# Kernel optimization log

Hardware: AMD Instinct MI355X
Metric: run time of the kernel (lower is better)

Reference implementation:

```python
import jax, jax.numpy as jnp
import numpy as np
from math import sqrt

B, N, D = 8, 4096, 512

def rotary(x, phases):
    # x: [B,N,D], phases: [B,N,D/2]
    c, s = jnp.cos(phases), jnp.sin(phases)
    a, b = jnp.split(x, 2, axis=-1)
    return jnp.concatenate([a * c - b * s, a * s + b * c], axis=-1)

def setup_inputs() -> dict:
    key = jax.random.key(0)
    ks = jax.random.split(key, 8)
    phi = jax.random.normal(ks[0], (B, N, D), dtype=jnp.float32)
    coords = jax.random.normal(ks[1], (B, N, 3), dtype=jnp.float32)
    weights = jax.random.uniform(ks[2], (B, N), dtype=jnp.float32)
    std = 1.0 / sqrt(D)
    Wq = jax.random.normal(ks[3], (D, D), dtype=jnp.float32) * std
    Wk = jax.random.normal(ks[4], (D, D), dtype=jnp.float32) * std
    Wv = jax.random.normal(ks[5], (D, D), dtype=jnp.float32) * std
    bq = jnp.zeros((D,), jnp.float32)
    bk = jnp.zeros((D,), jnp.float32)
    bv = jnp.zeros((D,), jnp.float32)
    # mode_lift weight, std = 1/kernel_scale with kernel_scale=1.0
    Wrot = jax.random.normal(ks[6], (D // 2, 3), dtype=jnp.float32)
    return {"phi": phi, "coords": coords, "weights": weights,
            "Wq": Wq, "bq": bq, "Wk": Wk, "bk": bk, "Wv": Wv, "bv": bv,
            "Wrot": Wrot}

def reference(phi, coords, weights, Wq, bq, Wk, bk, Wv, bv, Wrot):
    d = phi.shape[-1]
    q = phi @ Wq.T + bq
    k = phi @ Wk.T + bk
    v = phi @ Wv.T + bv
    # _normalize: scale query by 1/sqrt(d); attach quadrature weights to value
    q = q * (1.0 / sqrt(d))
    v = weights[..., None] * v
    # rotary positional encoding on q and k
    phases = jnp.einsum('bnc,dc->bnd', coords, Wrot)  # [B,N,D/2]
    q = rotary(q, phases)
    k = rotary(k, phases)
    # linear attention: q @ (k^T @ v), O(N*d^2)
    kv = jnp.einsum('bnd,bne->bde', k, v)   # [B,D,D]
    return jnp.einsum('bnd,bde->bne', q, kv)  # [B,N,D]
```

## Files before the change

### kernel.cpp

```cpp
#include <hip/hip_runtime.h>


typedef _Float16 f16x8 __attribute__((ext_vector_type(8)));
typedef _Float16 f16x4 __attribute__((ext_vector_type(4)));
typedef float f32x4 __attribute__((ext_vector_type(4)));

__device__ __forceinline__ void gl_lds16(const void* g, void* l) {
    __builtin_amdgcn_global_load_lds(
        (const __attribute__((address_space(1))) void*)g,
        (__attribute__((address_space(3))) void*)l, 16, 0, 0);
}

__device__ __forceinline__ void stage2(const _Float16* gA, size_t sA,
                                       const _Float16* gB, size_t sB,
                                       _Float16* As, _Float16* Bs,
                                       int ca, int srow, int sseg) {
    gl_lds16(&gA[(size_t)(ca * 16 + srow) * sA + sseg], &As[ca * 512]);
    gl_lds16(&gA[(size_t)(ca * 16 + 16 + srow) * sA + sseg], &As[(ca + 1) * 512]);
    gl_lds16(&gB[(size_t)(ca * 16 + srow) * sB + sseg], &Bs[ca * 512]);
    gl_lds16(&gB[(size_t)(ca * 16 + 16 + srow) * sB + sseg], &Bs[(ca + 1) * 512]);
}

__device__ __forceinline__ void mfma_step(const _Float16* As, const _Float16* Bs,
                                          int wm, int wn, int l16, int quad,
                                          f32x4 acc[4][4]) {
    f16x8 af[4], bf[4];
    #pragma unroll
    for (int mi = 0; mi < 4; mi++)
        af[mi] = *(const f16x8*)&As[(wm + mi * 16 + l16) * 32 + quad * 8];
    #pragma unroll
    for (int ni = 0; ni < 4; ni++)
        bf[ni] = *(const f16x8*)&Bs[(wn + ni * 16 + l16) * 32 + quad * 8];
    #pragma unroll
    for (int mi = 0; mi < 4; mi++)
        #pragma unroll
        for (int ni = 0; ni < 4; ni++)
            acc[mi][ni] = __builtin_amdgcn_mfma_f32_16x16x32_f16(
                af[mi], bf[ni], acc[mi][ni], 0, 0, 0);
}

__global__ __launch_bounds__(256) void convert_phi(const float* __restrict__ phi,
                                                   _Float16* __restrict__ phi_h) {
    int i = (blockIdx.x * 256 + threadIdx.x) * 4;
    float4 v = *(const float4*)(phi + i);
    f16x4 o = {(_Float16)v.x, (_Float16)v.y, (_Float16)v.z, (_Float16)v.w};
    *(f16x4*)(phi_h + i) = o;
}

__global__ __launch_bounds__(256) void pack_w(
    const float* __restrict__ Wq, const float* __restrict__ Wk,
    const float* __restrict__ Wv, const float* __restrict__ bq,
    const float* __restrict__ bk, const float* __restrict__ bv,
    _Float16* __restrict__ wcat, float* __restrict__ bcat) {
    int j = blockIdx.x;
    int reg = j >> 9, jr = j & 511;
    const float* W; const float* bias;
    if (reg == 0)      { W = Wq; bias = bq; }
    else if (reg == 1) { W = Wk; bias = bk; }
    else               { W = Wv; bias = bv; }
    int d = (reg < 2) ? ((jr & 1) ? (jr >> 1) + 256 : (jr >> 1)) : jr;
    for (int i = threadIdx.x; i < 512; i += 256)
        wcat[j * 512 + i] = (_Float16)W[d * 512 + i];
    if (threadIdx.x == 0) bcat[j] = bias[d];
}

__global__ __launch_bounds__(256) void qkv_kernel(
    const _Float16* __restrict__ phi_h, const _Float16* __restrict__ wcat,
    const float* __restrict__ bcat, const float* __restrict__ coords,
    const float* __restrict__ weights, const float* __restrict__ Wrot,
    _Float16* __restrict__ qr, _Float16* __restrict__ krT,
    _Float16* __restrict__ vwT) {
    __shared__ __align__(16) char smem[34816];
    _Float16* As0 = (_Float16*)smem;
    _Float16* Bs0 = (_Float16*)(smem + 8192);
    _Float16* As1 = (_Float16*)(smem + 16384);
    _Float16* Bs1 = (_Float16*)(smem + 24576);
    _Float16* Ts  = (_Float16*)smem;

    const int tid = threadIdx.x;
    const int lane = tid & 63, wave = tid >> 6;
    const int quad = lane >> 4, l16 = lane & 15;
    const int wm = (wave >> 1) * 64, wn = (wave & 1) * 64;
    const int m0 = blockIdx.y * 128;
    const int c0 = blockIdx.x * 128;
    const int ca = wave * 2;
    const int srow = lane >> 2, sseg = (lane & 3) * 8;

    const _Float16* gA = phi_h + (size_t)m0 * 512;
    const _Float16* gB = wcat + (size_t)c0 * 512;

    f32x4 acc[4][4] = {};

    stage2(gA, 512, gB, 512, As0, Bs0, ca, srow, sseg);
    __syncthreads();
    for (int k0 = 0; k0 < 512; k0 += 64) {
        stage2(gA + k0 + 32, 512, gB + k0 + 32, 512, As1, Bs1, ca, srow, sseg);
        mfma_step(As0, Bs0, wm, wn, l16, quad, acc);
        __syncthreads();
        if (k0 + 64 < 512)
            stage2(gA + k0 + 64, 512, gB + k0 + 64, 512, As0, Bs0, ca, srow, sseg);
        mfma_step(As1, Bs1, wm, wn, l16, quad, acc);
        __syncthreads();
    }

    const int region = c0 >> 9;
    const float qscale = 0.04419417382415922f;

    float bias[4], w0[4], w1[4], w2[4];
    #pragma unroll
    for (int ni = 0; ni < 4; ni++) {
        int gc = c0 + wn + ni * 16 + l16;
        bias[ni] = bcat[gc];
        if (region < 2) {
            int jp = (gc & 511) >> 1;
            w0[ni] = Wrot[jp * 3];
            w1[ni] = Wrot[jp * 3 + 1];
            w2[ni] = Wrot[jp * 3 + 2];
        }
    }

    if (region == 0) {
        #pragma unroll
        for (int mi = 0; mi < 4; mi++)
            #pragma unroll
            for (int r = 0; r < 4; r++) {
                int row = wm + mi * 16 + quad * 4 + r;
                int gm = m0 + row;
                float x = coords[gm * 3], y = coords[gm * 3 + 1], z = coords[gm * 3 + 2];
                #pragma unroll
                for (int ni = 0; ni < 4; ni++) {
                    float val = (acc[mi][ni][r] + bias[ni]) * qscale;
                    float part = __shfl_xor(val, 1);
                    float ph = x * w0[ni] + y * w1[ni] + z * w2[ni];
                    float sv, cv; __sincosf(ph, &sv, &cv);
                    float res = (l16 & 1) ? (part * sv + val * cv)
                                          : (val * cv - part * sv);
                    Ts[row * 136 + wn + ni * 16 + l16] = (_Float16)res;
                }
            }
        __syncthreads();
        for (int i = tid; i < 2048; i += 256) {
            int row = i >> 4, cv = (i & 15) * 8;
            *(f16x8*)&qr[(m0 + row) * 512 + c0 + cv] = *(f16x8*)&Ts[row * 136 + cv];
        }
    } else {
        #pragma unroll
        for (int mi = 0; mi < 4; mi++)
            #pragma unroll
            for (int r = 0; r < 4; r++) {
                int row = wm + mi * 16 + quad * 4 + r;
                int gm = m0 + row;
                if (region == 1) {
                    float x = coords[gm * 3], y = coords[gm * 3 + 1], z = coords[gm * 3 + 2];
                    #pragma unroll
                    for (int ni = 0; ni < 4; ni++) {
                        float val = acc[mi][ni][r] + bias[ni];
                        float part = __shfl_xor(val, 1);
                        float ph = x * w0[ni] + y * w1[ni] + z * w2[ni];
                        float sv, cv; __sincosf(ph, &sv, &cv);
                        float res = (l16 & 1) ? (part * sv + val * cv)
                                              : (val * cv - part * sv);
                        Ts[(wn + ni * 16 + l16) * 136 + row] = (_Float16)res;
                    }
                } else {
                    float wgt = weights[gm];
                    #pragma unroll
                    for (int ni = 0; ni < 4; ni++) {
                        float val = (acc[mi][ni][r] + bias[ni]) * wgt;
                        Ts[(wn + ni * 16 + l16) * 136 + row] = (_Float16)val;
                    }
                }
            }
        __syncthreads();
        _Float16* dst = (region == 1) ? krT : vwT;
        const int b = m0 >> 12, n0 = m0 & 4095, cb = c0 & 511;
        for (int i = tid; i < 2048; i += 256) {
            int col = i >> 4, rv = (i & 15) * 8;
            *(f16x8*)&dst[((size_t)b * 512 + cb + col) * 4096 + n0 + rv] =
                *(f16x8*)&Ts[col * 136 + rv];
        }
    }
}

__global__ __launch_bounds__(256) void kv_kernel(
    const _Float16* __restrict__ vwT, const _Float16* __restrict__ krT,
    _Float16* __restrict__ kvp) {
    __shared__ __align__(16) char smem[32768];
    _Float16* As0 = (_Float16*)smem;
    _Float16* Bs0 = (_Float16*)(smem + 8192);
    _Float16* As1 = (_Float16*)(smem + 16384);
    _Float16* Bs1 = (_Float16*)(smem + 24576);
    const int tid = threadIdx.x, lane = tid & 63, wave = tid >> 6;
    const int quad = lane >> 4, l16 = lane & 15;
    const int wm = (wave >> 1) * 64, wn = (wave & 1) * 64;
    const int d0 = blockIdx.x * 128, e0 = blockIdx.y * 128;
    const int b = blockIdx.z >> 3, split = blockIdx.z & 7;
    const int ca = wave * 2;
    const int srow = lane >> 2, sseg = (lane & 3) * 8;
    const size_t base = (size_t)b * 512 * 4096;
    const int kbeg = split * 512;
    const _Float16* gA = vwT + base + (size_t)e0 * 4096 + kbeg;
    const _Float16* gB = krT + base + (size_t)d0 * 4096 + kbeg;
    f32x4 acc[4][4] = {};

    stage2(gA, 4096, gB, 4096, As0, Bs0, ca, srow, sseg);
    __syncthreads();
    for (int k0 = 0; k0 < 512; k0 += 64) {
        stage2(gA + k0 + 32, 4096, gB + k0 + 32, 4096, As1, Bs1, ca, srow, sseg);
        mfma_step(As0, Bs0, wm, wn, l16, quad, acc);
        __syncthreads();
        if (k0 + 64 < 512)
            stage2(gA + k0 + 64, 4096, gB + k0 + 64, 4096, As0, Bs0, ca, srow, sseg);
        mfma_step(As1, Bs1, wm, wn, l16, quad, acc);
        __syncthreads();
    }

    _Float16* dst = kvp + ((size_t)split * 8 + b) * 262144;
    #pragma unroll
    for (int mi = 0; mi < 4; mi++)
        #pragma unroll
        for (int ni = 0; ni < 4; ni++)
            #pragma unroll
            for (int r = 0; r < 4; r++) {
                int e = e0 + wm + mi * 16 + quad * 4 + r;
                int d = d0 + wn + ni * 16 + l16;
                dst[e * 512 + d] = (_Float16)acc[mi][ni][r];
            }
}

__global__ __launch_bounds__(256) void reduce_kv(const _Float16* __restrict__ kvp,
                                                 _Float16* __restrict__ kvT) {
    int i = (blockIdx.x * 256 + threadIdx.x) * 8;
    float s[8] = {};
    #pragma unroll
    for (int sp = 0; sp < 8; sp++) {
        f16x8 v = *(const f16x8*)(kvp + (size_t)sp * 2097152 + i);
        #pragma unroll
        for (int j = 0; j < 8; j++) s[j] += (float)v[j];
    }
    f16x8 o;
    #pragma unroll
    for (int j = 0; j < 8; j++) o[j] = (_Float16)s[j];
    *(f16x8*)(kvT + i) = o;
}

__global__ __launch_bounds__(256) void out_kernel(
    const _Float16* __restrict__ qr, const _Float16* __restrict__ kvT,
    float* __restrict__ out) {
    __shared__ __align__(16) char smem[32768];
    _Float16* As0 = (_Float16*)smem;
    _Float16* Bs0 = (_Float16*)(smem + 8192);
    _Float16* As1 = (_Float16*)(smem + 16384);
    _Float16* Bs1 = (_Float16*)(smem + 24576);
    const int tid = threadIdx.x, lane = tid & 63, wave = tid >> 6;
    const int quad = lane >> 4, l16 = lane & 15;
    const int wm = (wave >> 1) * 64, wn = (wave & 1) * 64;
    const int m0 = blockIdx.y * 128, e0 = blockIdx.x * 128;
    const int b = m0 >> 12;
    const int ca = wave * 2;
    const int srow = lane >> 2, sseg = (lane & 3) * 8;
    const _Float16* gA = qr + (size_t)m0 * 512;
    const _Float16* gB = kvT + (size_t)b * 262144 + (size_t)e0 * 512;
    f32x4 acc[4][4] = {};

    stage2(gA, 512, gB, 512, As0, Bs0, ca, srow, sseg);
    __syncthreads();
    for (int k0 = 0; k0 < 512; k0 += 64) {
        stage2(gA + k0 + 32, 512, gB + k0 + 32, 512, As1, Bs1, ca, srow, sseg);
        mfma_step(As0, Bs0, wm, wn, l16, quad, acc);
        __syncthreads();
        if (k0 + 64 < 512)
            stage2(gA + k0 + 64, 512, gB + k0 + 64, 512, As0, Bs0, ca, srow, sseg);
        mfma_step(As1, Bs1, wm, wn, l16, quad, acc);
        __syncthreads();
    }

    #pragma unroll
    for (int mi = 0; mi < 4; mi++)
        #pragma unroll
        for (int ni = 0; ni < 4; ni++)
            #pragma unroll
            for (int r = 0; r < 4; r++) {
                int gm = m0 + wm + mi * 16 + quad * 4 + r;
                int e = e0 + wn + ni * 16 + l16;
                out[(size_t)gm * 512 + e] = acc[mi][ni][r];
            }
}

extern "C" void kernel_launch(void* const* d_in, const int* in_sizes, int n_in,
                              void* d_out, int out_size, void* d_ws, size_t ws_size,
                              hipStream_t stream) {
    const float* phi     = (const float*)d_in[0];
    const float* coords  = (const float*)d_in[1];
    const float* weights = (const float*)d_in[2];
    const float* Wq      = (const float*)d_in[3];
    const float* bq      = (const float*)d_in[4];
    const float* Wk      = (const float*)d_in[5];
    const float* bk      = (const float*)d_in[6];
    const float* Wv      = (const float*)d_in[7];
    const float* bv      = (const float*)d_in[8];
    const float* Wrot    = (const float*)d_in[9];
    float* out = (float*)d_out;

    char* ws = (char*)d_ws;
    _Float16* phi_h = (_Float16*)(ws);
    _Float16* kvp   = (_Float16*)(ws);
    _Float16* wcat  = (_Float16*)(ws + 33554432);
    float*    bcat  = (float*)   (ws + 35127296);
    _Float16* qr    = (_Float16*)(ws + 35133440);
    _Float16* krT   = (_Float16*)(ws + 68687872);
    _Float16* vwT   = (_Float16*)(ws + 102242304);
    _Float16* kvT   = (_Float16*)(ws + 135796736);

    convert_phi<<<16384, 256, 0, stream>>>(phi, phi_h);
    pack_w<<<1536, 256, 0, stream>>>(Wq, Wk, Wv, bq, bk, bv, wcat, bcat);
    qkv_kernel<<<dim3(12, 256), 256, 0, stream>>>(phi_h, wcat, bcat, coords,
                                                  weights, Wrot, qr, krT, vwT);
    kv_kernel<<<dim3(4, 4, 64), 256, 0, stream>>>(vwT, krT, kvp);
    reduce_kv<<<1024, 256, 0, stream>>>(kvp, kvT);
    out_kernel<<<dim3(4, 256), 256, 0, stream>>>(qr, kvT, out);
}
```

Before: 322.4 us.

## Swizzle LDS tiles and use vmcnt-gated double-buffer pipeline in GEMMs

Applies an XOR swizzle to the 16-byte segment index used by the global-to-LDS staging loads and the MFMA fragment reads, to reduce LDS bank conflicts. It also replaces the __syncthreads-based double-buffer loop with a fully unrolled pipeline. That pipeline issues two stages ahead, waits on vmcnt for only the oldest stage, and uses raw s_barrier with sched_barrier fences. The aim is to keep global loads in flight across MFMA steps. The hand-written waitcnt and barrier ordering adds fragility if the vmcnt count does not match the number of outstanding loads.

Result: faster. 310.9 us (-3.6%).

```diff
diff --git a/kernel.cpp b/kernel.cpp
--- a/kernel.cpp
+++ b/kernel.cpp
@@ -22,15 +22,15 @@
 }
 
 __device__ __forceinline__ void mfma_step(const _Float16* As, const _Float16* Bs,
-                                          int wm, int wn, int l16, int quad,
+                                          int wm, int wn, int l16, int qs,
                                           f32x4 acc[4][4]) {
     f16x8 af[4], bf[4];
     #pragma unroll
     for (int mi = 0; mi < 4; mi++)
-        af[mi] = *(const f16x8*)&As[(wm + mi * 16 + l16) * 32 + quad * 8];
+        af[mi] = *(const f16x8*)&As[(wm + mi * 16 + l16) * 32 + qs * 8];
     #pragma unroll
     for (int ni = 0; ni < 4; ni++)
-        bf[ni] = *(const f16x8*)&Bs[(wn + ni * 16 + l16) * 32 + quad * 8];
+        bf[ni] = *(const f16x8*)&Bs[(wn + ni * 16 + l16) * 32 + qs * 8];
     #pragma unroll
     for (int mi = 0; mi < 4; mi++)
         #pragma unroll
@@ -38,6 +38,36 @@
             acc[mi][ni] = __builtin_amdgcn_mfma_f32_16x16x32_f16(
                 af[mi], bf[ni], acc[mi][ni], 0, 0, 0);
 }
+
+#define PHASE(BUFA, BUFB, VM)                                                 \
+    asm volatile("s_waitcnt vmcnt(" #VM ")" ::: "memory");                    \
+    __builtin_amdgcn_s_barrier();                                             \
+    asm volatile("" ::: "memory");                                            \
+    __builtin_amdgcn_sched_barrier(0);                                        \
+    mfma_step(BUFA, BUFB, wm, wn, l16, qs, acc);                              \
+    asm volatile("s_waitcnt lgkmcnt(0)" ::: "memory");                        \
+    __builtin_amdgcn_sched_barrier(0);                                        \
+    __builtin_amdgcn_s_barrier();                                             \
+    asm volatile("" ::: "memory");
+
+#define PIPE_LOOP(gA, sA, gB, sB)                                             \
+    stage2(gA, sA, gB, sB, As0, Bs0, ca, srow, sseg);                         \
+    stage2(gA + 32, sA, gB + 32, sB, As1, Bs1, ca, srow, sseg);               \
+    _Pragma("unroll")                                                         \
+    for (int p = 0; p < 8; p++) {                                             \
+        const int t0 = 2 * p;                                                 \
+        PHASE(As0, Bs0, 4)                                                    \
+        if (t0 + 2 < 16)                                                      \
+            stage2(gA + (size_t)(t0 + 2) * 32, sA,                            \
+                   gB + (size_t)(t0 + 2) * 32, sB,                            \
+                   As0, Bs0, ca, srow, sseg);                                 \
+        if (p < 7) { PHASE(As1, Bs1, 4) }                                     \
+        else       { PHASE(As1, Bs1, 0) }                                     \
+        if (t0 + 3 < 16)                                                      \
+            stage2(gA + (size_t)(t0 + 3) * 32, sA,                            \
+                   gB + (size_t)(t0 + 3) * 32, sB,                            \
+                   As1, Bs1, ca, srow, sseg);                                 \
+    }
 
 __global__ __launch_bounds__(256) void convert_phi(const float* __restrict__ phi,
                                                    _Float16* __restrict__ phi_h) {
@@ -80,28 +110,20 @@
     const int tid = threadIdx.x;
     const int lane = tid & 63, wave = tid >> 6;
     const int quad = lane >> 4, l16 = lane & 15;
+    const int qs = quad ^ ((l16 >> 1) & 3);
     const int wm = (wave >> 1) * 64, wn = (wave & 1) * 64;
     const int m0 = blockIdx.y * 128;
     const int c0 = blockIdx.x * 128;
     const int ca = wave * 2;
-    const int srow = lane >> 2, sseg = (lane & 3) * 8;
+    const int srow = lane >> 2;
+    const int sseg = (((lane & 3) ^ ((lane >> 3) & 3)) * 8);
 
     const _Float16* gA = phi_h + (size_t)m0 * 512;
     const _Float16* gB = wcat + (size_t)c0 * 512;
 
     f32x4 acc[4][4] = {};
 
-    stage2(gA, 512, gB, 512, As0, Bs0, ca, srow, sseg);
-    __syncthreads();
-    for (int k0 = 0; k0 < 512; k0 += 64) {
-        stage2(gA + k0 + 32, 512, gB + k0 + 32, 512, As1, Bs1, ca, srow, sseg);
-        mfma_step(As0, Bs0, wm, wn, l16, quad, acc);
-        __syncthreads();
-        if (k0 + 64 < 512)
-            stage2(gA + k0 + 64, 512, gB + k0 + 64, 512, As0, Bs0, ca, srow, sseg);
-        mfma_step(As1, Bs1, wm, wn, l16, quad, acc);
-        __syncthreads();
-    }
+    PIPE_LOOP(gA, 512, gB, 512)
 
     const int region = c0 >> 9;
     const float qscale = 0.04419417382415922f;
@@ -192,28 +214,20 @@
     _Float16* Bs1 = (_Float16*)(smem + 24576);
     const int tid = threadIdx.x, lane = tid & 63, wave = tid >> 6;
     const int quad = lane >> 4, l16 = lane & 15;
+    const int qs = quad ^ ((l16 >> 1) & 3);
     const int wm = (wave >> 1) * 64, wn = (wave & 1) * 64;
     const int d0 = blockIdx.x * 128, e0 = blockIdx.y * 128;
     const int b = blockIdx.z >> 3, split = blockIdx.z & 7;
     const int ca = wave * 2;
-    const int srow = lane >> 2, sseg = (lane & 3) * 8;
+    const int srow = lane >> 2;
+    const int sseg = (((lane & 3) ^ ((lane >> 3) & 3)) * 8);
     const size_t base = (size_t)b * 512 * 4096;
     const int kbeg = split * 512;
     const _Float16* gA = vwT + base + (size_t)e0 * 4096 + kbeg;
     const _Float16* gB = krT + base + (size_t)d0 * 4096 + kbeg;
     f32x4 acc[4][4] = {};
 
-    stage2(gA, 4096, gB, 4096, As0, Bs0, ca, srow, sseg);
-    __syncthreads();
-    for (int k0 = 0; k0 < 512; k0 += 64) {
-        stage2(gA + k0 + 32, 4096, gB + k0 + 32, 4096, As1, Bs1, ca, srow, sseg);
-        mfma_step(As0, Bs0, wm, wn, l16, quad, acc);
-        __syncthreads();
-        if (k0 + 64 < 512)
-            stage2(gA + k0 + 64, 4096, gB + k0 + 64, 4096, As0, Bs0, ca, srow, sseg);
-        mfma_step(As1, Bs1, wm, wn, l16, quad, acc);
-        __syncthreads();
-    }
+    PIPE_LOOP(gA, 4096, gB, 4096)
 
     _Float16* dst = kvp + ((size_t)split * 8 + b) * 262144;
     #pragma unroll
@@ -254,26 +268,18 @@
     _Float16* Bs1 = (_Float16*)(smem + 24576);
     const int tid = threadIdx.x, lane = tid & 63, wave = tid >> 6;
     const int quad = lane >> 4, l16 = lane & 15;
+    const int qs = quad ^ ((l16 >> 1) & 3);
     const int wm = (wave >> 1) * 64, wn = (wave & 1) * 64;
     const int m0 = blockIdx.y * 128, e0 = blockIdx.x * 128;
     const int b = m0 >> 12;
     const int ca = wave * 2;
-    const int srow = lane >> 2, sseg = (lane & 3) * 8;
+    const int srow = lane >> 2;
+    const int sseg = (((lane & 3) ^ ((lane >> 3) & 3)) * 8);
     const _Float16* gA = qr + (size_t)m0 * 512;
     const _Float16* gB = kvT + (size_t)b * 262144 + (size_t)e0 * 512;
     f32x4 acc[4][4] = {};
 
-    stage2(gA, 512, gB, 512, As0, Bs0, ca, srow, sseg);
-    __syncthreads();
-    for (int k0 = 0; k0 < 512; k0 += 64) {
-        stage2(gA + k0 + 32, 512, gB + k0 + 32, 512, As1, Bs1, ca, srow, sseg);
-        mfma_step(As0, Bs0, wm, wn, l16, quad, acc);
-        __syncthreads();
-        if (k0 + 64 < 512)
-            stage2(gA + k0 + 64, 512, gB + k0 + 64, 512, As0, Bs0, ca, srow, sseg);
-        mfma_step(As1, Bs1, wm, wn, l16, quad, acc);
-        __syncthreads();
-    }
+    PIPE_LOOP(gA, 512, gB, 512)
 
     #pragma unroll
     for (int mi = 0; mi < 4; mi++)
```
